# Optimization experiments

Measured on AMD Instinct MI355X. Metric: run time of the kernel, lower is better.

## Reference

```python
import jax, jax.numpy as jnp
import numpy as np

T, B, I, H = 256, 128, 256, 1024
G = 4 * H  # LSTM gate size
PI_MIX, SIGMA1, SIGMA2 = 0.75, 1.0, 0.001


def _gauss_logpdf(x, mu, sigma):
    z = (x - mu) / sigma
    return -0.5 * z * z - jnp.log(sigma) - 0.5 * jnp.log(2.0 * jnp.pi)


def _compute_kl(x, mu, sigma):
    log_post = jnp.sum(_gauss_logpdf(x, mu, sigma))
    mix1 = jnp.sum(_gauss_logpdf(x, 0.0, SIGMA1)) + jnp.log(PI_MIX)
    mix2 = jnp.sum(_gauss_logpdf(x, 0.0, SIGMA2)) + jnp.log(1.0 - PI_MIX)
    log_prior = jnp.logaddexp(mix1, mix2)
    return log_post - log_prior


def setup_inputs() -> dict:
    key = jax.random.key(0)
    ks = jax.random.split(key, 13)
    u = lambda k, shape, lo, hi: jax.random.uniform(k, shape, jnp.float32, lo, hi)
    return {
        "x": jax.random.normal(ks[0], (T, B, I), jnp.float32),
        "w_ih_mu": u(ks[1], (G, I), -0.05, 0.05),
        "w_ih_rho": u(ks[2], (G, I), -4.0, -1.0),
        "w_hh_mu": u(ks[3], (G, H), -0.05, 0.05),
        "w_hh_rho": u(ks[4], (G, H), -4.0, -1.0),
        "b_ih_mu": u(ks[5], (G,), -0.05, 0.05),
        "b_ih_rho": u(ks[6], (G,), -4.0, -1.0),
        "b_hh_mu": u(ks[7], (G,), -0.05, 0.05),
        "b_hh_rho": u(ks[8], (G,), -4.0, -1.0),
        "eps_w_ih": jax.random.normal(ks[9], (G, I), jnp.float32),
        "eps_w_hh": jax.random.normal(ks[10], (G, H), jnp.float32),
        "eps_b_ih": jax.random.normal(ks[11], (G,), jnp.float32),
        "eps_b_hh": jax.random.normal(ks[12], (G,), jnp.float32),
    }


def reference(x, w_ih_mu, w_ih_rho, w_hh_mu, w_hh_rho,
              b_ih_mu, b_ih_rho, b_hh_mu, b_hh_rho,
              eps_w_ih, eps_w_hh, eps_b_ih, eps_b_hh):
    # Bayes-by-backprop weight sampling: w = mu + eps * (softplus(rho) + 1e-5)
    s_w_ih = jax.nn.softplus(w_ih_rho) + 1e-5
    s_w_hh = jax.nn.softplus(w_hh_rho) + 1e-5
    s_b_ih = jax.nn.softplus(b_ih_rho) + 1e-5
    s_b_hh = jax.nn.softplus(b_hh_rho) + 1e-5
    w_ih = w_ih_mu + eps_w_ih * s_w_ih  # [4H, I]
    w_hh = w_hh_mu + eps_w_hh * s_w_hh  # [4H, H]
    b_ih = b_ih_mu + eps_b_ih * s_b_ih  # [4H]
    b_hh = b_hh_mu + eps_b_hh * s_b_hh  # [4H]

    kl = (_compute_kl(w_ih, w_ih_mu, s_w_ih)
          + _compute_kl(w_hh, w_hh_mu, s_w_hh)
          + _compute_kl(b_ih, b_ih_mu, s_b_ih)
          + _compute_kl(b_hh, b_hh_mu, s_b_hh))

    # Precompute input projections for all timesteps: [T, B, 4H]
    x_proj = jnp.einsum('tbi,gi->tbg', x, w_ih) + b_ih + b_hh

    h0 = jnp.zeros((B, H), x.dtype)
    c0 = jnp.zeros((B, H), x.dtype)

    def step(carry, xp_t):
        h, c = carry
        gates = xp_t + h @ w_hh.T  # [B, 4H]
        i_g, f_g, g_g, o_g = jnp.split(gates, 4, axis=-1)  # PyTorch gate order i,f,g,o
        c_new = jax.nn.sigmoid(f_g) * c + jax.nn.sigmoid(i_g) * jnp.tanh(g_g)
        h_new = jax.nn.sigmoid(o_g) * jnp.tanh(c_new)
        return (h_new, c_new), h_new

    (h_n, c_n), output = jax.lax.scan(step, (h0, c0), x_proj)
    return output, h_n[None], c_n[None], kl
```

## Files before the change

kernel.cpp:

```cpp
#include <hip/hip_runtime.h>
#include <hip/hip_bf16.h>

typedef unsigned short u16;
typedef __attribute__((ext_vector_type(8))) short short8;
typedef __attribute__((ext_vector_type(4))) float f32x4;

#define T_STEPS 256
#define BATCH   128
#define ISIZE   256
#define HSIZE   1024
#define GSIZE   4096
#define KCAT    1280

#define WCAT_OFF  0UL
#define XBF_OFF   10485760UL
#define ABUF_OFF  27262976UL
#define BCOMB_OFF 27918336UL
#define SUMS_OFF  27934720UL
#define FLAG_OFF  27934848UL
#define XCC_OFF   27935872UL

#define OUT_ELEMS ((size_t)T_STEPS * BATCH * HSIZE)
#define HN_OFF    (OUT_ELEMS)
#define CN_OFF    (OUT_ELEMS + (size_t)BATCH * HSIZE)
#define KL_OFF    (OUT_ELEMS + 2UL * BATCH * HSIZE)

static __device__ __forceinline__ u16 f2bf(float f) {
  union { __hip_bfloat16 h; u16 u; } cv;
  cv.h = __float2bfloat16(f);
  return cv.u;
}

static __device__ __forceinline__ f32x4 mfma16(short8 a, short8 b, f32x4 c) {
  return __builtin_amdgcn_mfma_f32_16x16x32_bf16(a, b, c, 0, 0, 0);
}

static __device__ __forceinline__ float sigm(float v) {
  return 1.0f / (1.0f + __expf(-v));
}
static __device__ __forceinline__ float tanh_(float v) {
  v = fminf(12.0f, fmaxf(-12.0f, v));
  float e = __expf(2.0f * v);
  return (e - 1.0f) / (e + 1.0f);
}

static __device__ void block_reduce_atomic(const float* v, int n, double* dst) {
  __shared__ float red[6][4];
  float loc[6];
  for (int i = 0; i < n; ++i) loc[i] = v[i];
#pragma unroll
  for (int off = 32; off > 0; off >>= 1)
    for (int i = 0; i < n; ++i) loc[i] += __shfl_down(loc[i], off, 64);
  __syncthreads();
  const int wv = threadIdx.x >> 6, ln = threadIdx.x & 63;
  if (ln == 0)
    for (int i = 0; i < n; ++i) red[i][wv] = loc[i];
  __syncthreads();
  if (threadIdx.x == 0)
    for (int i = 0; i < n; ++i)
      atomicAdd(dst + i, (double)(red[i][0] + red[i][1] + red[i][2] + red[i][3]));
  __syncthreads();
}

__global__ __launch_bounds__(256) void prep_kernel(
    const float* __restrict__ x,
    const float* __restrict__ wih_mu, const float* __restrict__ wih_rho,
    const float* __restrict__ whh_mu, const float* __restrict__ whh_rho,
    const float* __restrict__ bih_mu, const float* __restrict__ bih_rho,
    const float* __restrict__ bhh_mu, const float* __restrict__ bhh_rho,
    const float* __restrict__ eih, const float* __restrict__ ehh,
    const float* __restrict__ ebi, const float* __restrict__ ebh,
    u16* __restrict__ wcat, u16* __restrict__ xbf,
    float* __restrict__ bcomb, double* __restrict__ sums)
{
  const unsigned stride = gridDim.x * blockDim.x;
  const unsigned tid0 = blockIdx.x * blockDim.x + threadIdx.x;
  float s[6];

  s[0] = s[1] = s[2] = 0.f;
  for (unsigned i = tid0; i < GSIZE * ISIZE; i += stride) {
    float mu = wih_mu[i], rho = wih_rho[i], ep = eih[i];
    float sg = log1pf(__expf(rho)) + 1e-5f;
    float w  = fmaf(ep, sg, mu);
    unsigned g = i >> 8, k = i & 255u;
    wcat[(size_t)g * KCAT + HSIZE + k] = f2bf(w);
    s[0] += ep * ep; s[1] += __logf(sg); s[2] += w * w;
  }
  block_reduce_atomic(s, 3, sums + 0);

  s[0] = s[1] = s[2] = 0.f;
  for (unsigned i = tid0; i < GSIZE * HSIZE; i += stride) {
    float mu = whh_mu[i], rho = whh_rho[i], ep = ehh[i];
    float sg = log1pf(__expf(rho)) + 1e-5f;
    float w  = fmaf(ep, sg, mu);
    unsigned g = i >> 10, k = i & 1023u;
    wcat[(size_t)g * KCAT + k] = f2bf(w);
    s[0] += ep * ep; s[1] += __logf(sg); s[2] += w * w;
  }
  block_reduce_atomic(s, 3, sums + 3);

  for (int i = 0; i < 6; ++i) s[i] = 0.f;
  for (unsigned i = tid0; i < GSIZE; i += stride) {
    float mu = bih_mu[i], rho = bih_rho[i], ep = ebi[i];
    float sg = log1pf(__expf(rho)) + 1e-5f;
    float w  = fmaf(ep, sg, mu);
    s[0] += ep * ep; s[1] += __logf(sg); s[2] += w * w;
    float mu2 = bhh_mu[i], rho2 = bhh_rho[i], ep2 = ebh[i];
    float sg2 = log1pf(__expf(rho2)) + 1e-5f;
    float w2  = fmaf(ep2, sg2, mu2);
    s[3] += ep2 * ep2; s[4] += __logf(sg2); s[5] += w2 * w2;
    bcomb[i] = w + w2;
  }
  block_reduce_atomic(s, 6, sums + 6);

  for (unsigned i = tid0; i < (unsigned)T_STEPS * BATCH * ISIZE; i += stride)
    xbf[i] = f2bf(x[i]);
}

__global__ void kl_finalize(const double* __restrict__ sums, float* __restrict__ out_kl) {
  const double LOG2PI = 1.8378770664093453;
  const double Ns[4] = {1048576.0, 4194304.0, 4096.0, 4096.0};
  double kl = 0.0;
#pragma unroll
  for (int t = 0; t < 4; ++t) {
    double S1 = sums[t * 3 + 0], S2 = sums[t * 3 + 1], S3 = sums[t * 3 + 2];
    double N = Ns[t];
    double log_post = -0.5 * S1 - S2 - 0.5 * N * LOG2PI;
    double mix1 = -0.5 * S3 - 0.5 * N * LOG2PI + log(0.75);
    double mix2 = -0.5 * S3 * 1.0e6 - N * log(1.0e-3) - 0.5 * N * LOG2PI + log(0.25);
    double mx = fmax(mix1, mix2), mn = fmin(mix1, mix2);
    double log_prior = mx + log1p(exp(mn - mx));
    kl += log_post - log_prior;
  }
  *out_kl = (float)kl;
}

static __device__ __forceinline__ short8 loadA16(const u16* p) {
  short8 r;
  asm volatile("global_load_dwordx4 %0, %1, off sc0" : "=&v"(r) : "v"(p));
  return r;
}

static __device__ __forceinline__ void publish_flag(unsigned* p, unsigned v, bool strong) {
  if (strong)
    __hip_atomic_store(p, v, __ATOMIC_RELEASE, __HIP_MEMORY_SCOPE_AGENT);
  else
    __hip_atomic_store(p, v, __ATOMIC_RELAXED, __HIP_MEMORY_SCOPE_AGENT);
}

static __device__ __forceinline__ void wait_group(const unsigned* f, unsigned target, bool strong) {
  const int lane = threadIdx.x & 63;
  unsigned v;
  do {
    v = (lane < 32) ? __hip_atomic_load(f + lane, __ATOMIC_RELAXED, __HIP_MEMORY_SCOPE_AGENT)
                    : target;
  } while (!__all((int)(v >= target)));
  if (strong)
    __builtin_amdgcn_fence(__ATOMIC_ACQUIRE, "agent");
}

__global__ __launch_bounds__(512, 2) void lstm_kernel(
    const u16* __restrict__ wcat, const u16* __restrict__ xbf,
    u16* __restrict__ abuf, const float* __restrict__ bcomb,
    float* __restrict__ out, unsigned* __restrict__ flags,
    unsigned* __restrict__ xccs)
{
  __shared__ float gates_p[8][16][128];

  const int tid  = threadIdx.x;
  const int wv   = tid >> 6;
  const int lane = tid & 63;
  const int col  = lane & 15;
  const int ksub = lane >> 4;
  const int bm   = blockIdx.x & 7;
  const int bj   = blockIdx.x >> 3;
  const int j0   = bj << 5;
  const int b0   = bm << 4;
  const int wsw  = (ksub & 1) << 4;

  unsigned* gflags = flags + bm * 32;

  unsigned xcc;
  asm volatile("s_getreg_b32 %0, hwreg(20, 0, 32)" : "=s"(xcc));
  xcc = (xcc & 15u) + 1u;
  if (tid == 0)
    __hip_atomic_store(xccs + blockIdx.x, xcc, __ATOMIC_RELAXED, __HIP_MEMORY_SCOPE_AGENT);
  bool strong;
  {
    unsigned mine = 0, head = 0;
    int filled;
    do {
      filled = 1;
      if (tid < 256) {
        mine = __hip_atomic_load(xccs + tid, __ATOMIC_RELAXED, __HIP_MEMORY_SCOPE_AGENT);
        head = __hip_atomic_load(xccs + (tid & 7), __ATOMIC_RELAXED, __HIP_MEMORY_SCOPE_AGENT);
        filled = (mine != 0u) && (head != 0u);
      }
    } while (!__syncthreads_and(filled));
    int match = (tid < 256) ? (mine == head) : 1;
    strong = !__syncthreads_and(match);
  }

  short8 wfrag[5][8];
#pragma unroll
  for (int i = 0; i < 5; ++i) {
    const int kk = wv * 5 + i;
#pragma unroll
    for (int n = 0; n < 8; ++n) {
      const int rowg = ((n >> 1) << 10) + j0 + ((n & 1) << 4) + col;
      wfrag[i][n] = *(const short8*)(wcat + (size_t)rowg * KCAT + (kk << 5) + (ksub << 3));
    }
  }
  float bias[8];
#pragma unroll
  for (int n = 0; n < 8; ++n)
    bias[n] = bcomb[((n >> 1) << 10) + j0 + ((n & 1) << 4) + col];

  const int bl = tid >> 5;
  const int jj = tid & 31;
  const int rsw = ((bl >> 2) & 1) << 4;
  float creg = 0.f;

  if (bj == 0) {
    const int row = tid >> 5, seg = tid & 31;
    short8 v = *(const short8*)(xbf + ((size_t)(b0 + row)) * ISIZE + (seg << 3));
    *(short8*)(abuf + (size_t)(b0 + row) * KCAT + HSIZE + (seg << 3)) = v;
  }
  __syncthreads();
  if (tid == 0) publish_flag(gflags + bj, 1u, strong);

  for (int t = 0; t < T_STEPS; ++t) {
    const u16* curA = abuf + (size_t)(t & 1) * (BATCH * KCAT);
    u16*       nxtA = abuf + (size_t)((t & 1) ^ 1) * (BATCH * KCAT);

    if (wv == 0) wait_group(gflags, (unsigned)(t + 1), strong);
    __syncthreads();

    if (!strong) asm volatile("buffer_inv" ::: "memory");

    short8 av[5];
    const u16* aptr = curA + (size_t)(b0 + col) * KCAT + ((wv * 5) << 5) + (ksub << 3);
#pragma unroll
    for (int i = 0; i < 5; ++i) av[i] = loadA16(aptr + (i << 5));
    asm volatile("s_waitcnt vmcnt(0)" ::: "memory");
    __builtin_amdgcn_sched_barrier(0);

    f32x4 acc[8] = {};
#pragma unroll
    for (int i = 0; i < 5; ++i)
#pragma unroll
      for (int n = 0; n < 8; ++n)
        acc[n] = mfma16(av[i], wfrag[i][n], acc[n]);

    if (wv == 0) {
#pragma unroll
      for (int n = 0; n < 8; ++n) {
        acc[n][0] += bias[n]; acc[n][1] += bias[n];
        acc[n][2] += bias[n]; acc[n][3] += bias[n];
      }
    }
#pragma unroll
    for (int n = 0; n < 8; ++n)
#pragma unroll
      for (int v = 0; v < 4; ++v)
        gates_p[wv][ksub * 4 + v][((n << 4) + col) ^ wsw] = acc[n][v];
    __syncthreads();

    {
      float gi = 0.f, gf = 0.f, gg = 0.f, go = 0.f;
#pragma unroll
      for (int w = 0; w < 8; ++w) {
        gi += gates_p[w][bl][jj ^ rsw];
        gf += gates_p[w][bl][(32 + jj) ^ rsw];
        gg += gates_p[w][bl][(64 + jj) ^ rsw];
        go += gates_p[w][bl][(96 + jj) ^ rsw];
      }
      float ig = sigm(gi), fg = sigm(gf), og = sigm(go);
      float cn = fg * creg + ig * tanh_(gg);
      creg = cn;
      float h = og * tanh_(cn);
      size_t hidx = (size_t)(b0 + bl) * HSIZE + (size_t)(j0 + jj);
      out[(size_t)t * (BATCH * HSIZE) + hidx] = h;
      nxtA[(size_t)(b0 + bl) * KCAT + (j0 + jj)] = f2bf(h);
      if (t == T_STEPS - 1) {
        out[HN_OFF + hidx] = h;
        out[CN_OFF + hidx] = cn;
      }
    }
    if (bj == 0 && t + 1 < T_STEPS) {
      const int row = tid >> 5, seg = tid & 31;
      short8 v = *(const short8*)(xbf + ((size_t)(t + 1) * BATCH + b0 + row) * ISIZE + (seg << 3));
      *(short8*)(nxtA + (size_t)(b0 + row) * KCAT + HSIZE + (seg << 3)) = v;
    }
    __syncthreads();
    if (tid == 0 && t + 1 < T_STEPS)
      publish_flag(gflags + bj, (unsigned)(t + 2), strong);
  }
}

extern "C" void kernel_launch(void* const* d_in, const int* in_sizes, int n_in,
                              void* d_out, int out_size, void* d_ws, size_t ws_size,
                              hipStream_t stream) {
  (void)in_sizes; (void)n_in; (void)out_size; (void)ws_size;
  const float* x       = (const float*)d_in[0];
  const float* wih_mu  = (const float*)d_in[1];
  const float* wih_rho = (const float*)d_in[2];
  const float* whh_mu  = (const float*)d_in[3];
  const float* whh_rho = (const float*)d_in[4];
  const float* bih_mu  = (const float*)d_in[5];
  const float* bih_rho = (const float*)d_in[6];
  const float* bhh_mu  = (const float*)d_in[7];
  const float* bhh_rho = (const float*)d_in[8];
  const float* eih     = (const float*)d_in[9];
  const float* ehh     = (const float*)d_in[10];
  const float* ebi     = (const float*)d_in[11];
  const float* ebh     = (const float*)d_in[12];

  float* out = (float*)d_out;
  char* ws = (char*)d_ws;
  u16* wcat    = (u16*)(ws + WCAT_OFF);
  u16* xbf     = (u16*)(ws + XBF_OFF);
  u16* abuf    = (u16*)(ws + ABUF_OFF);
  float* bcomb = (float*)(ws + BCOMB_OFF);
  double* sums = (double*)(ws + SUMS_OFF);
  unsigned* flags = (unsigned*)(ws + FLAG_OFF);
  unsigned* xccs  = (unsigned*)(ws + XCC_OFF);

  hipMemsetAsync(ws + SUMS_OFF, 0, 2176, stream);
  hipMemsetAsync(ws + ABUF_OFF, 0, 2UL * BATCH * KCAT * 2, stream);

  prep_kernel<<<512, 256, 0, stream>>>(x, wih_mu, wih_rho, whh_mu, whh_rho,
      bih_mu, bih_rho, bhh_mu, bhh_rho, eih, ehh, ebi, ebh, wcat, xbf, bcomb, sums);
  kl_finalize<<<1, 1, 0, stream>>>(sums, out + KL_OFF);
  lstm_kernel<<<256, 512, 0, stream>>>(wcat, xbf, abuf, bcomb, out, flags, xccs);
}
```

Before: 1.085 ms.

## Wait per-wave on only needed h slices and read x directly

```diff
diff --git a/kernel.cpp b/kernel.cpp
--- a/kernel.cpp
+++ b/kernel.cpp
@@ -148,11 +148,12 @@
     __hip_atomic_store(p, v, __ATOMIC_RELAXED, __HIP_MEMORY_SCOPE_AGENT);
 }
 
-static __device__ __forceinline__ void wait_group(const unsigned* f, unsigned target, bool strong) {
+static __device__ __forceinline__ void wait_slices(const unsigned* f, int nf,
+                                                   unsigned target, bool strong) {
   const int lane = threadIdx.x & 63;
   unsigned v;
   do {
-    v = (lane < 32) ? __hip_atomic_load(f + lane, __ATOMIC_RELAXED, __HIP_MEMORY_SCOPE_AGENT)
+    v = (lane < nf) ? __hip_atomic_load(f + lane, __ATOMIC_RELAXED, __HIP_MEMORY_SCOPE_AGENT)
                     : target;
   } while (!__all((int)(v >= target)));
   if (strong)
@@ -179,6 +180,8 @@
   const int wsw  = (ksub & 1) << 4;
 
   unsigned* gflags = flags + bm * 32;
+  const int sbase = wv * 5;
+  int nf = 32 - sbase; if (nf > 5) nf = 5; if (nf < 0) nf = 0;
 
   unsigned xcc;
   asm volatile("s_getreg_b32 %0, hwreg(20, 0, 32)" : "=s"(xcc));
@@ -204,7 +207,7 @@
   short8 wfrag[5][8];
 #pragma unroll
   for (int i = 0; i < 5; ++i) {
-    const int kk = wv * 5 + i;
+    const int kk = sbase + i;
 #pragma unroll
     for (int n = 0; n < 8; ++n) {
       const int rowg = ((n >> 1) << 10) + j0 + ((n & 1) << 4) + col;
@@ -221,27 +224,26 @@
   const int rsw = ((bl >> 2) & 1) << 4;
   float creg = 0.f;
 
-  if (bj == 0) {
-    const int row = tid >> 5, seg = tid & 31;
-    short8 v = *(const short8*)(xbf + ((size_t)(b0 + row)) * ISIZE + (seg << 3));
-    *(short8*)(abuf + (size_t)(b0 + row) * KCAT + HSIZE + (seg << 3)) = v;
-  }
-  __syncthreads();
   if (tid == 0) publish_flag(gflags + bj, 1u, strong);
 
   for (int t = 0; t < T_STEPS; ++t) {
-    const u16* curA = abuf + (size_t)(t & 1) * (BATCH * KCAT);
-    u16*       nxtA = abuf + (size_t)((t & 1) ^ 1) * (BATCH * KCAT);
-
-    if (wv == 0) wait_group(gflags, (unsigned)(t + 1), strong);
-    __syncthreads();
-
-    if (!strong) asm volatile("buffer_inv" ::: "memory");
+    const u16* curA = abuf + (size_t)(t & 1) * (BATCH * HSIZE);
+    u16*       nxtA = abuf + (size_t)((t & 1) ^ 1) * (BATCH * HSIZE);
+
+    if (nf > 0) {
+      wait_slices(gflags + sbase, nf, (unsigned)(t + 1), strong);
+      if (!strong) asm volatile("buffer_inv" ::: "memory");
+    }
 
     short8 av[5];
-    const u16* aptr = curA + (size_t)(b0 + col) * KCAT + ((wv * 5) << 5) + (ksub << 3);
-#pragma unroll
-    for (int i = 0; i < 5; ++i) av[i] = loadA16(aptr + (i << 5));
+    const u16* hbase = curA + (size_t)(b0 + col) * HSIZE + (ksub << 3);
+    const u16* xbase = xbf + ((size_t)t * BATCH + b0 + col) * ISIZE + (ksub << 3);
+#pragma unroll
+    for (int i = 0; i < 5; ++i) {
+      const int kk = sbase + i;
+      const u16* p = (kk < 32) ? (hbase + (kk << 5)) : (xbase + ((kk - 32) << 5));
+      av[i] = loadA16(p);
+    }
     asm volatile("s_waitcnt vmcnt(0)" ::: "memory");
     __builtin_amdgcn_sched_barrier(0);
 
@@ -266,6 +268,7 @@
         gates_p[wv][ksub * 4 + v][((n << 4) + col) ^ wsw] = acc[n][v];
     __syncthreads();
 
+    float h, cn;
     {
       float gi = 0.f, gf = 0.f, gg = 0.f, go = 0.f;
 #pragma unroll
@@ -276,25 +279,24 @@
         go += gates_p[w][bl][(96 + jj) ^ rsw];
       }
       float ig = sigm(gi), fg = sigm(gf), og = sigm(go);
-      float cn = fg * creg + ig * tanh_(gg);
+      cn = fg * creg + ig * tanh_(gg);
       creg = cn;
-      float h = og * tanh_(cn);
+      h = og * tanh_(cn);
+      nxtA[(size_t)(b0 + bl) * HSIZE + (j0 + jj)] = f2bf(h);
+    }
+    __syncthreads();
+
+    if (tid == 0 && t + 1 < T_STEPS)
+      publish_flag(gflags + bj, (unsigned)(t + 2), strong);
+
+    {
       size_t hidx = (size_t)(b0 + bl) * HSIZE + (size_t)(j0 + jj);
       out[(size_t)t * (BATCH * HSIZE) + hidx] = h;
-      nxtA[(size_t)(b0 + bl) * KCAT + (j0 + jj)] = f2bf(h);
       if (t == T_STEPS - 1) {
         out[HN_OFF + hidx] = h;
         out[CN_OFF + hidx] = cn;
       }
     }
-    if (bj == 0 && t + 1 < T_STEPS) {
-      const int row = tid >> 5, seg = tid & 31;
-      short8 v = *(const short8*)(xbf + ((size_t)(t + 1) * BATCH + b0 + row) * ISIZE + (seg << 3));
-      *(short8*)(nxtA + (size_t)(b0 + row) * KCAT + HSIZE + (seg << 3)) = v;
-    }
-    __syncthreads();
-    if (tid == 0 && t + 1 < T_STEPS)
-      publish_flag(gflags + bj, (unsigned)(t + 2), strong);
   }
 }
 
@@ -327,7 +329,7 @@
   unsigned* xccs  = (unsigned*)(ws + XCC_OFF);
 
   hipMemsetAsync(ws + SUMS_OFF, 0, 2176, stream);
-  hipMemsetAsync(ws + ABUF_OFF, 0, 2UL * BATCH * KCAT * 2, stream);
+  hipMemsetAsync(ws + ABUF_OFF, 0, 2UL * BATCH * HSIZE * 2, stream);
 
   prep_kernel<<<512, 256, 0, stream>>>(x, wih_mu, wih_rho, whh_mu, whh_rho,
       bih_mu, bih_rho, bhh_mu, bhh_rho, eih, ehh, ebi, ebh, wcat, xbf, bcomb, sums);
```

Result: slower. 1.451 ms (+33.8%).
